# Optimization experiments

Hardware: AMD Instinct MI355X
Metric: run time of the kernel (lower is better)

Reference implementation:

```python
import jax, jax.numpy as jnp
import numpy as np

B, L, D, H, NL, DFF = 32, 64, 256, 8, 2, 2048
S, I, DSEM, DDENSE, DSPARSE = 16, 16, 128, 128, 128


def layer_norm(x, g, b, eps=1e-5):
    m = x.mean(-1, keepdims=True)
    v = ((x - m) ** 2).mean(-1, keepdims=True)
    return (x - m) / jnp.sqrt(v + eps) * g + b


def encoder_layer(x, ipw, ipb, ow, ob, g1, b1, g2, b2, f1w, f1b, f2w, f2b):
    # PyTorch TransformerEncoderLayer (post-norm, ReLU FFN, dropout inactive).
    b, t, d = x.shape
    dh = d // H
    qkv = x @ ipw.T + ipb  # (b,t,3d)
    q, k, v = jnp.split(qkv, 3, axis=-1)
    split_heads = lambda z: z.reshape(b, t, H, dh).transpose(0, 2, 1, 3)
    q, k, v = split_heads(q), split_heads(k), split_heads(v)
    att = jax.nn.softmax(jnp.einsum('bhqd,bhkd->bhqk', q, k) / np.float32(np.sqrt(dh)), axis=-1)
    o = jnp.einsum('bhqk,bhkd->bhqd', att, v).transpose(0, 2, 1, 3).reshape(b, t, d)
    x = layer_norm(x + o @ ow.T + ob, g1, b1)
    h = jax.nn.relu(x @ f1w.T + f1b) @ f2w.T + f2b
    return layer_norm(x + h, g2, b2)


def setup_inputs() -> dict:
    key = jax.random.key(0)
    ks = jax.random.split(key, 16)
    sc = np.float32(0.02)
    return dict(
        dense=jax.random.normal(ks[0], (B, L, DDENSE), jnp.float32),
        sparse=jax.random.normal(ks[1], (B, L, DSPARSE), jnp.float32),
        W_feat=jax.random.normal(ks[2], (DDENSE + DSPARSE, D), jnp.float32) * sc,
        b_feat=jnp.zeros((D,), jnp.float32),
        in_proj_w=jax.random.normal(ks[3], (NL, 3 * D, D), jnp.float32) * sc,
        in_proj_b=jnp.zeros((NL, 3 * D), jnp.float32),
        out_w=jax.random.normal(ks[4], (NL, D, D), jnp.float32) * sc,
        out_b=jnp.zeros((NL, D), jnp.float32),
        ln1_g=jnp.ones((NL, D), jnp.float32), ln1_b=jnp.zeros((NL, D), jnp.float32),
        ln2_g=jnp.ones((NL, D), jnp.float32), ln2_b=jnp.zeros((NL, D), jnp.float32),
        ff1_w=jax.random.normal(ks[5], (NL, DFF, D), jnp.float32) * sc,
        ff1_b=jnp.zeros((NL, DFF), jnp.float32),
        ff2_w=jax.random.normal(ks[6], (NL, D, DFF), jnp.float32) * sc,
        ff2_b=jnp.zeros((NL, D), jnp.float32),
        w_act=jax.random.normal(ks[7], (D, 1), jnp.float32) * sc,
        w_route_ws=jax.random.normal(ks[8], (L, S, D), jnp.float32) * sc,
        w_pose_ws=jax.random.normal(ks[9], (L, S, D, D), jnp.float32) * sc,
        w_route_si=jax.random.normal(ks[10], (S, I, D), jnp.float32) * sc,
        w_pose_si=jax.random.normal(ks[11], (S, I, D, D), jnp.float32) * sc,
        cls_w=jax.random.normal(ks[12], (DSEM, 2 * D), jnp.float32) * sc,
        cls_b=jnp.zeros((DSEM,), jnp.float32),
        inorm_g=jnp.ones((DSEM,), jnp.float32),
        inorm_b=jnp.zeros((DSEM,), jnp.float32),
    )


def reference(dense, sparse, W_feat, b_feat, in_proj_w, in_proj_b, out_w, out_b,
              ln1_g, ln1_b, ln2_g, ln2_b, ff1_w, ff1_b, ff2_w, ff2_b,
              w_act, w_route_ws, w_pose_ws, w_route_si, w_pose_si,
              cls_w, cls_b, inorm_g, inorm_b):
    # TokenFeaturizer: concat(dense, sparse) -> Linear -> (b,L,d)
    tok = jnp.concatenate([dense, sparse], axis=-1) @ W_feat + b_feat
    cls = tok.sum(axis=1, keepdims=True)  # einsum 'bld->bd' CLS token
    x = jnp.concatenate([tok, cls], axis=1)  # (b, L+1, d)
    for i in range(in_proj_w.shape[0]):
        x = encoder_layer(x, in_proj_w[i], in_proj_b[i], out_w[i], out_b[i],
                          ln1_g[i], ln1_b[i], ln2_g[i], ln2_b[i],
                          ff1_w[i], ff1_b[i], ff2_w[i], ff2_b[i])
    words, cls_tok = x[:, :L], x[:, L]  # (b,L,d), (b,d)

    # --- route words -> slots ('weighted_sig') ---
    a_words = jax.nn.sigmoid((words @ w_act)[..., 0])  # (b,L)
    c_ws = jax.nn.softmax(jnp.einsum('lsd,bld->bls', w_route_ws, words), axis=-1)
    a_num = jnp.einsum('bls,bl->bs', c_ws, a_words)
    a_slots = a_num / a_words.sum(axis=1, keepdims=True)
    u_hat = jnp.einsum('lsij,blj->blsi', w_pose_ws, words)  # (b,L,S,d)
    u_num = jnp.einsum('bls,bl,blsi->bsi', c_ws, a_words, u_hat)
    u_slots = u_num / a_num[..., None]  # (b,S,d)

    # --- route slots -> intents ---
    c_si = jax.nn.softmax(jnp.einsum('sid,bsd->bsi', w_route_si, u_slots), axis=-1)
    an = jnp.einsum('bsi,bs->bi', c_si, a_slots)
    a_intents = an / (a_slots.sum(axis=1, keepdims=True) + 1e-8)
    u_hat_i = jnp.einsum('sijk,bsk->bsik', w_pose_si, u_slots)  # (b,S,I,d)
    un = jnp.einsum('bsi,bs,bsik->bik', c_si, a_slots, u_hat_i)
    u_intents = un / (an[..., None] + 1e-8)  # (b,I,d)

    # argmax over intents, gather winning pose
    idx = jnp.argmax(a_intents, axis=-1)  # (b,)
    poses = u_intents[jnp.arange(u_intents.shape[0]), idx]  # (b,d)
    intents = jnp.concatenate([cls_tok, poses], axis=-1) @ cls_w.T + cls_b
    intents = layer_norm(intents, inorm_g, inorm_b)
    return (c_ws, intents)
```

## Files before the change

### kernel.cpp

```cpp
#include <hip/hip_runtime.h>
#include <hip/hip_bf16.h>
#include <math.h>

#define B_ 32
#define L_ 64
#define D_ 256
#define H_ 8
#define T_ 65
#define NT_ (B_*T_)
#define DFF_ 2048
#define S_ 16
#define I_ 16
#define DSEM_ 128

typedef __attribute__((ext_vector_type(8))) short bf16x8;
typedef __attribute__((ext_vector_type(4))) float f32x4;

typedef __attribute__((address_space(1))) const void gbl_void;
typedef __attribute__((address_space(3))) void lds_void;
#define GLOAD16(g, l) __builtin_amdgcn_global_load_lds((gbl_void*)(g), (lds_void*)(l), 16, 0, 0)

__device__ inline unsigned short f2bu(float f) {
  union { float f; unsigned u; } a; a.f = f;
  unsigned r = a.u + 0x7FFF + ((a.u >> 16) & 1);
  return (unsigned short)(r >> 16);
}
__device__ inline float b2f(unsigned short u) {
  union { unsigned u; float f; } a; a.u = ((unsigned)u) << 16;
  return a.f;
}

__device__ inline float wave_reduce_sum(float v) {
#pragma unroll
  for (int m = 32; m >= 1; m >>= 1) v += __shfl_xor(v, m, 64);
  return v;
}

__device__ inline float block_reduce_sum_256(float v, float* sred) {
  v = wave_reduce_sum(v);
  int tid = threadIdx.x;
  if ((tid & 63) == 0) sred[tid >> 6] = v;
  __syncthreads();
  float r = sred[0] + sred[1] + sred[2] + sred[3];
  __syncthreads();
  return r;
}

__global__ __launch_bounds__(256) void conv_fused_kernel(
    const float* __restrict__ dense, const float* __restrict__ sparse, unsigned short* __restrict__ cat,
    const float* __restrict__ wfeat, unsigned short* __restrict__ wfeatT,
    const float* __restrict__ ipw, const float* __restrict__ ow,
    const float* __restrict__ f1w, const float* __restrict__ f2w,
    unsigned short* __restrict__ ipwB, unsigned short* __restrict__ owB,
    unsigned short* __restrict__ f1wB, unsigned short* __restrict__ f2wB) {
  __shared__ float tb[64][65];
  int bid = blockIdx.x, tid = threadIdx.x;
  if (bid < 2048) {
    int idx = bid * 256 + tid;
    int r = idx >> 8, c = idx & 255;
    float v = (c < 128) ? dense[r * 128 + c] : sparse[r * 128 + (c - 128)];
    cat[idx] = f2bu(v);
  } else if (bid < 2064) {
    int blk = bid - 2048;
    int k0 = (blk & 3) * 64, n0 = (blk >> 2) * 64;
    int wid = tid >> 6, lane = tid & 63;
#pragma unroll
    for (int p = 0; p < 16; ++p)
      tb[p * 4 + wid][lane] = wfeat[(size_t)(k0 + p * 4 + wid) * 256 + n0 + lane];
    __syncthreads();
#pragma unroll
    for (int p = 0; p < 16; ++p)
      wfeatT[(size_t)(n0 + p * 4 + wid) * 256 + k0 + lane] = f2bu(tb[lane][p * 4 + wid]);
  } else {
    int i = (bid - 2064) * 256 + tid;
    const float* src; unsigned short* dst; int off;
    if (i < 98304)       { src = ipw; dst = ipwB; off = i; }
    else if (i < 131072) { src = ow;  dst = owB;  off = i - 98304; }
    else if (i < 393216) { src = f1w; dst = f1wB; off = i - 131072; }
    else                 { src = f2w; dst = f2wB; off = i - 393216; }
    float4 v = ((const float4*)src)[off];
    short4 o;
    o.x = (short)f2bu(v.x); o.y = (short)f2bu(v.y);
    o.z = (short)f2bu(v.z); o.w = (short)f2bu(v.w);
    ((short4*)dst)[off] = o;
  }
}

template <int ACT, int OUT_BF16, int NFRAG>
__global__ __launch_bounds__(256) void gemm_bf2_kernel(const unsigned short* __restrict__ A,
                                                       const unsigned short* __restrict__ W,
                                                       const float* __restrict__ bias,
                                                       float* __restrict__ Cf, unsigned short* __restrict__ Cb,
                                                       int M, int N, int K) {
  __shared__ __align__(16) unsigned short As[2][32 * 64];
  __shared__ __align__(16) unsigned short Bs[2][NFRAG * 64 * 64];
  int tid = threadIdx.x, wid = tid >> 6, lane = tid & 63;
  int row0 = blockIdx.y * 32, col0 = blockIdx.x * (64 * NFRAG);
  int lr = lane >> 3;
  int sc = ((lane & 7) ^ (lr & 7)) << 3;
  const unsigned short* Asrc = A + (size_t)(row0 + wid * 8 + lr) * K + sc;
  const unsigned short* Bsrc[2 * NFRAG];
#pragma unroll
  for (int p = 0; p < 2 * NFRAG; ++p)
    Bsrc[p] = W + (size_t)(col0 + wid * 16 * NFRAG + p * 8 + lr) * K + sc;
  unsigned short* AsW = &As[0][0] + wid * (8 * 64);
  unsigned short* BsW = &Bs[0][0] + wid * (16 * NFRAG * 64);

  f32x4 acc[2][NFRAG];
#pragma unroll
  for (int i = 0; i < 2; ++i)
#pragma unroll
    for (int j = 0; j < NFRAG; ++j) acc[i][j] = (f32x4){0.f, 0.f, 0.f, 0.f};

  GLOAD16(Asrc, AsW);
#pragma unroll
  for (int p = 0; p < 2 * NFRAG; ++p) GLOAD16(Bsrc[p], BsW + p * (8 * 64));

  int nk = K >> 6, cur = 0;
  int kg = lane >> 4, l15 = lane & 15;
  for (int kt = 0; kt < nk; ++kt) {
    __syncthreads();
    if (kt + 1 < nk) {
      int k0 = (kt + 1) << 6;
      GLOAD16(Asrc + k0, AsW + (cur ^ 1) * (32 * 64));
#pragma unroll
      for (int p = 0; p < 2 * NFRAG; ++p)
        GLOAD16(Bsrc[p] + k0, BsW + (cur ^ 1) * (NFRAG * 64 * 64) + p * (8 * 64));
    }
    const unsigned short* Ab = &As[cur][0];
    const unsigned short* Bb = &Bs[cur][0];
#pragma unroll
    for (int kk = 0; kk < 2; ++kk) {
      int cc = kk * 4 + kg;
      bf16x8 bfr[NFRAG];
#pragma unroll
      for (int fn = 0; fn < NFRAG; ++fn) {
        int rn = wid * 16 * NFRAG + fn * 16 + l15;
        bfr[fn] = *(const bf16x8*)&Bb[rn * 64 + ((cc ^ (rn & 7)) << 3)];
      }
#pragma unroll
      for (int fm = 0; fm < 2; ++fm) {
        int rm = fm * 16 + l15;
        bf16x8 afr = *(const bf16x8*)&Ab[rm * 64 + ((cc ^ (rm & 7)) << 3)];
#pragma unroll
        for (int fn = 0; fn < NFRAG; ++fn)
          acc[fm][fn] = __builtin_amdgcn_mfma_f32_16x16x32_bf16(afr, bfr[fn], acc[fm][fn], 0, 0, 0);
      }
    }
    cur ^= 1;
  }
#pragma unroll
  for (int fm = 0; fm < 2; ++fm) {
#pragma unroll
    for (int fn = 0; fn < NFRAG; ++fn) {
      int col = col0 + wid * 16 * NFRAG + fn * 16 + l15;
      float bi = bias[col];
      int rbase = row0 + fm * 16 + ((lane >> 4) << 2);
#pragma unroll
      for (int r = 0; r < 4; ++r) {
        int grow = rbase + r;
        float v = acc[fm][fn][r] + bi;
        if (ACT == 1) v = fmaxf(v, 0.f);
        if (OUT_BF16) Cb[(size_t)grow * N + col] = f2bu(v);
        else          Cf[(size_t)grow * N + col] = v;
      }
    }
  }
}

__global__ __launch_bounds__(256) void ln_residual_kernel(float* __restrict__ x, unsigned short* __restrict__ xbf,
                                                          const float* __restrict__ proj,
                                                          const float* __restrict__ g, const float* __restrict__ bb) {
  __shared__ float sred[4];
  int r = blockIdx.x, d = threadIdx.x;
  float v = x[(size_t)r * D_ + d] + proj[(size_t)r * D_ + d];
  float mean = block_reduce_sum_256(v, sred) * (1.f / 256.f);
  float dv = v - mean;
  float var = block_reduce_sum_256(dv * dv, sred) * (1.f / 256.f);
  float o = dv * (1.f / sqrtf(var + 1e-5f)) * g[d] + bb[d];
  x[(size_t)r * D_ + d] = o;
  xbf[(size_t)r * D_ + d] = f2bu(o);
}

__global__ void build_x_kernel(const float* __restrict__ tok, float* __restrict__ x,
                               unsigned short* __restrict__ xbf) {
  int b = blockIdx.x, d = threadIdx.x;
  float s = 0.f;
  for (int l = 0; l < L_; ++l) {
    float v = tok[((size_t)(b * L_ + l)) * D_ + d];
    size_t o = ((size_t)(b * T_ + l)) * D_ + d;
    x[o] = v; xbf[o] = f2bu(v);
    s += v;
  }
  size_t o = ((size_t)(b * T_ + L_)) * D_ + d;
  x[o] = s; xbf[o] = f2bu(s);
}

__global__ __launch_bounds__(256) void attn_kernel(const unsigned short* __restrict__ qkv,
                                                   unsigned short* __restrict__ attn_out) {
  int bh = blockIdx.x;
  int b = bh >> 3, h = bh & 7;
  __shared__ float Q[T_][32], K[T_][32], V[T_][32];
  __shared__ float Sc[T_][T_ + 1];
  int tid = threadIdx.x;
  for (int idx = tid; idx < T_ * 32; idx += 256) {
    int t = idx >> 5, d = idx & 31;
    const unsigned short* base = qkv + ((size_t)(b * T_ + t)) * 768 + h * 32 + d;
    Q[t][d] = b2f(base[0]);
    K[t][d] = b2f(base[256]);
    V[t][d] = b2f(base[512]);
  }
  __syncthreads();
  for (int idx = tid; idx < T_ * T_; idx += 256) {
    int qi = idx / T_, ki = idx % T_;
    float s = 0.f;
#pragma unroll
    for (int d = 0; d < 32; ++d) s += Q[qi][d] * K[ki][d];
    Sc[qi][ki] = s * 0.17677669529663687f;
  }
  __syncthreads();
  {
    int q = tid & 3;
    for (int row = tid >> 2; row < T_; row += 64) {
      float mx = -1e30f;
      for (int k = q; k < T_; k += 4) mx = fmaxf(mx, Sc[row][k]);
      mx = fmaxf(mx, __shfl_xor(mx, 1, 64));
      mx = fmaxf(mx, __shfl_xor(mx, 2, 64));
      float sum = 0.f;
      for (int k = q; k < T_; k += 4) { float e = expf(Sc[row][k] - mx); Sc[row][k] = e; sum += e; }
      sum += __shfl_xor(sum, 1, 64);
      sum += __shfl_xor(sum, 2, 64);
      float inv = 1.f / sum;
      for (int k = q; k < T_; k += 4) Sc[row][k] *= inv;
    }
  }
  __syncthreads();
  for (int idx = tid; idx < T_ * 32; idx += 256) {
    int t = idx >> 5, d = idx & 31;
    float acc = 0.f;
    for (int k = 0; k < T_; ++k) acc += Sc[t][k] * V[k][d];
    attn_out[((size_t)(b * T_ + t)) * D_ + h * 32 + d] = f2bu(acc);
  }
}

__global__ __launch_bounds__(256) void cws_kernel(const float* __restrict__ x, const float* __restrict__ w_route,
                                                  const float* __restrict__ w_act, float* __restrict__ c_ws_out,
                                                  float* __restrict__ a_words) {
  int bl = blockIdx.x;
  int b = bl >> 6, l = bl & 63;
  __shared__ float word[256];
  __shared__ float logits[16];
  __shared__ float sred[4];
  int t = threadIdx.x;
  word[t] = x[((size_t)(b * T_ + l)) * D_ + t];
  __syncthreads();
  float pa = word[t] * w_act[t];
  float asum = block_reduce_sum_256(pa, sred);
  if (t == 0) a_words[b * 64 + l] = 1.f / (1.f + expf(-asum));
  int s = t >> 4, j0 = t & 15;
  float p = 0.f;
  for (int j = j0; j < 256; j += 16) p += w_route[((size_t)(l * 16 + s)) * 256 + j] * word[j];
#pragma unroll
  for (int m = 8; m >= 1; m >>= 1) p += __shfl_xor(p, m, 64);
  if (j0 == 0) logits[s] = p;
  __syncthreads();
  if (t < 16) {
    float mx = -1e30f;
#pragma unroll
    for (int k = 0; k < 16; ++k) mx = fmaxf(mx, logits[k]);
    float sum = 0.f;
#pragma unroll
    for (int k = 0; k < 16; ++k) sum += expf(logits[k] - mx);
    c_ws_out[(size_t)bl * 16 + t] = expf(logits[t] - mx) / sum;
  }
}

__global__ __launch_bounds__(64) void slot_agg_kernel(const float* __restrict__ c_ws, const float* __restrict__ a_words,
                                                      float* __restrict__ a_num, float* __restrict__ a_slots,
                                                      float* __restrict__ asl_sum) {
  int b = blockIdx.x, lane = threadIdx.x;
  float aw = a_words[b * 64 + lane];
  float asum = wave_reduce_sum(aw);
  float inv = 1.f / asum;
  float ssum = 0.f;
  for (int s = 0; s < 16; ++s) {
    float p = c_ws[((size_t)(b * 64 + lane)) * 16 + s] * aw;
    float r = wave_reduce_sum(p);
    if (lane == 0) {
      a_num[b * 16 + s] = r;
      a_slots[b * 16 + s] = r * inv;
      ssum += r * inv;
    }
  }
  if (lane == 0) asl_sum[b] = ssum;
}

__global__ __launch_bounds__(256, 4) void pose_ws3_kernel(const unsigned short* __restrict__ xbf,
                                                          const float* __restrict__ P,
                                                          const float* __restrict__ c_ws,
                                                          const float* __restrict__ a_words,
                                                          float* __restrict__ partial) {
  int bid = blockIdx.x;
  int ih = bid & 1, s = (bid >> 1) & 15, lg = bid >> 5;
  int iBase = ih * 128;
  __shared__ __align__(16) unsigned short Bs[32 * 256];
  int tid = threadIdx.x, wid = tid >> 6, lane = tid & 63;
  int kg = lane >> 4, l15 = lane & 15;
  f32x4 acc[2][2];
#pragma unroll
  for (int i = 0; i < 2; ++i)
#pragma unroll
    for (int j = 0; j < 2; ++j) acc[i][j] = (f32x4){0.f, 0.f, 0.f, 0.f};

#pragma unroll
  for (int li = 0; li < 2; ++li) {
    int l = lg + li * 32;
    __syncthreads();
    {
      int b = tid >> 3, c0 = (tid & 7) * 4;
      float w = c_ws[((size_t)(b * 64 + l)) * 16 + s] * a_words[b * 64 + l];
      const unsigned short* src = xbf + ((size_t)(b * T_ + l)) * D_;
#pragma unroll
      for (int j = 0; j < 4; ++j) {
        int c = c0 + j;
        union { float4 f4; unsigned short u[8]; } in, out;
        in.f4 = *(const float4*)(src + c * 8);
#pragma unroll
        for (int e = 0; e < 8; ++e) out.u[e] = f2bu(w * b2f(in.u[e]));
        *(float4*)&Bs[b * 256 + ((c ^ (b & 7)) << 3)] = out.f4;
      }
    }
    __syncthreads();
    const float* Pbase = P + (((size_t)(l * 16 + s)) << 16);
#pragma unroll
    for (int k0 = 0; k0 < 256; k0 += 64) {
#pragma unroll
      for (int kk = 0; kk < 2; ++kk) {
        int cc = (k0 >> 3) + kk * 4 + kg;
        bf16x8 bfr[2];
#pragma unroll
        for (int fn = 0; fn < 2; ++fn) {
          int rb = fn * 16 + l15;
          bfr[fn] = *(const bf16x8*)&Bs[rb * 256 + ((cc ^ (rb & 7)) << 3)];
        }
        int kbase = k0 + kk * 32 + kg * 8;
#pragma unroll
        for (int fm = 0; fm < 2; ++fm) {
          int row = iBase + wid * 32 + fm * 16 + l15;
          const float* src = Pbase + (size_t)row * 256 + kbase;
          float4 v0 = *(const float4*)src;
          float4 v1 = *(const float4*)(src + 4);
          union { bf16x8 b8; unsigned short u[8]; } pk;
          pk.u[0] = f2bu(v0.x); pk.u[1] = f2bu(v0.y); pk.u[2] = f2bu(v0.z); pk.u[3] = f2bu(v0.w);
          pk.u[4] = f2bu(v1.x); pk.u[5] = f2bu(v1.y); pk.u[6] = f2bu(v1.z); pk.u[7] = f2bu(v1.w);
          acc[fm][0] = __builtin_amdgcn_mfma_f32_16x16x32_bf16(pk.b8, bfr[0], acc[fm][0], 0, 0, 0);
          acc[fm][1] = __builtin_amdgcn_mfma_f32_16x16x32_bf16(pk.b8, bfr[1], acc[fm][1], 0, 0, 0);
        }
      }
    }
  }
  float* pout = partial + ((size_t)(lg * 16 + s)) * 8192;
#pragma unroll
  for (int fm = 0; fm < 2; ++fm) {
#pragma unroll
    for (int fn = 0; fn < 2; ++fn) {
      int b = fn * 16 + l15;
      int i0 = iBase + wid * 32 + fm * 16 + (kg << 2);
#pragma unroll
      for (int r = 0; r < 4; ++r)
        pout[(i0 + r) * 32 + b] = acc[fm][fn][r];
    }
  }
}

__global__ __launch_bounds__(256) void reduce_uslots_kernel(const float* __restrict__ partial,
                                                            const float* __restrict__ a_num,
                                                            float* __restrict__ u_slots) {
  int s = blockIdx.x >> 5, ic = blockIdx.x & 31;
  int t = threadIdx.x;
  int i = ic * 8 + (t >> 5), b = t & 31;
  size_t off = (size_t)s * 8192 + i * 32 + b;
  float a0 = 0.f, a1 = 0.f, a2 = 0.f, a3 = 0.f;
#pragma unroll
  for (int lg = 0; lg < 32; lg += 4) {
    a0 += partial[((size_t)(lg + 0) * 16) * 8192 + off];
    a1 += partial[((size_t)(lg + 1) * 16) * 8192 + off];
    a2 += partial[((size_t)(lg + 2) * 16) * 8192 + off];
    a3 += partial[((size_t)(lg + 3) * 16) * 8192 + off];
  }
  u_slots[((size_t)(b * 16 + s)) * 256 + i] = (a0 + a1 + a2 + a3) / a_num[b * 16 + s];
}

__global__ __launch_bounds__(256) void csi_kernel(const float* __restrict__ u_slots, const float* __restrict__ w_route_si,
                                                  float* __restrict__ c_si) {
  int bs = blockIdx.x;
  int s = bs & 15;
  __shared__ float row[256];
  __shared__ float logits[16];
  int t = threadIdx.x;
  row[t] = u_slots[(size_t)bs * 256 + t];
  __syncthreads();
  int i = t >> 4, j0 = t & 15;
  float p = 0.f;
  for (int j = j0; j < 256; j += 16) p += w_route_si[((size_t)(s * 16 + i)) * 256 + j] * row[j];
#pragma unroll
  for (int m = 8; m >= 1; m >>= 1) p += __shfl_xor(p, m, 64);
  if (j0 == 0) logits[i] = p;
  __syncthreads();
  if (t < 16) {
    float mx = -1e30f;
#pragma unroll
    for (int k = 0; k < 16; ++k) mx = fmaxf(mx, logits[k]);
    float sum = 0.f;
#pragma unroll
    for (int k = 0; k < 16; ++k) sum += expf(logits[k] - mx);
    c_si[(size_t)bs * 16 + t] = expf(logits[t] - mx) / sum;
  }
}

__global__ void pose_si_partial_kernel(const float* __restrict__ P, float* __restrict__ R4) {
  int si = blockIdx.x >> 2, jc = blockIdx.x & 3;
  int k = threadIdx.x;
  const float* base = P + (size_t)si * 65536 + (size_t)jc * 64 * 256 + k;
  float a0 = 0.f, a1 = 0.f, a2 = 0.f, a3 = 0.f;
#pragma unroll
  for (int j = 0; j < 64; j += 4) {
    a0 += base[(j + 0) * 256];
    a1 += base[(j + 1) * 256];
    a2 += base[(j + 2) * 256];
    a3 += base[(j + 3) * 256];
  }
  R4[(size_t)jc * 65536 + si * 256 + k] = a0 + a1 + a2 + a3;
}

__global__ __launch_bounds__(256) void un_merged_kernel(const float* __restrict__ c_si,
                                                        const float* __restrict__ a_slots,
                                                        const float* __restrict__ R4,
                                                        const float* __restrict__ u_slots,
                                                        float* __restrict__ u_pose) {
  int b = blockIdx.x, t = threadIdx.x;
  __shared__ float csi_s[256];
  __shared__ float asl_s[16];
  __shared__ float an_s[16];
  __shared__ float w_s[16];
  __shared__ float an_star;
  __shared__ int istar_s;
  csi_s[t] = c_si[(size_t)b * 256 + t];
  if (t < 16) asl_s[t] = a_slots[b * 16 + t];
  __syncthreads();
  if (t < 16) {
    float acc = 0.f;
#pragma unroll
    for (int s = 0; s < 16; ++s) acc += csi_s[s * 16 + t] * asl_s[s];
    an_s[t] = acc;
  }
  __syncthreads();
  if (t == 0) {
    int best = 0;
    float bv = an_s[0];
    for (int k = 1; k < 16; ++k)
      if (an_s[k] > bv) { bv = an_s[k]; best = k; }
    istar_s = best;
    an_star = bv;
  }
  __syncthreads();
  int istar = istar_s;
  if (t < 16) w_s[t] = csi_s[t * 16 + istar] * asl_s[t];
  __syncthreads();
  float acc = 0.f;
#pragma unroll
  for (int s = 0; s < 16; ++s) {
    size_t ro = ((size_t)(s * 16 + istar)) * 256 + t;
    float r = R4[ro] + R4[65536 + ro] + R4[131072 + ro] + R4[196608 + ro];
    acc += w_s[s] * r * u_slots[((size_t)(b * 16 + s)) * 256 + t];
  }
  u_pose[(size_t)b * 256 + t] = acc / (an_star + 1e-8f);
}

__global__ __launch_bounds__(128) void final_kernel(const float* __restrict__ x, const float* __restrict__ u_pose,
                                                    const float* __restrict__ cls_w,
                                                    const float* __restrict__ cls_b, const float* __restrict__ g,
                                                    const float* __restrict__ bb, float* __restrict__ out) {
  int b = blockIdx.x, m = threadIdx.x;
  __shared__ float row[512];
  __shared__ float sred[2];
  for (int d = m; d < 256; d += 128) {
    row[d] = x[((size_t)(b * T_ + L_)) * D_ + d];
    row[256 + d] = u_pose[(size_t)b * 256 + d];
  }
  __syncthreads();
  float acc = cls_b[m];
  for (int j = 0; j < 512; ++j) acc += cls_w[(size_t)m * 512 + j] * row[j];
  float v = wave_reduce_sum(acc);
  if ((m & 63) == 0) sred[m >> 6] = v;
  __syncthreads();
  float mean = (sred[0] + sred[1]) * (1.f / 128.f);
  __syncthreads();
  float dv = acc - mean;
  float v2 = wave_reduce_sum(dv * dv);
  if ((m & 63) == 0) sred[m >> 6] = v2;
  __syncthreads();
  float var = (sred[0] + sred[1]) * (1.f / 128.f);
  out[(size_t)b * 128 + m] = dv * (1.f / sqrtf(var + 1e-5f)) * g[m] + bb[m];
}

extern "C" void kernel_launch(void* const* d_in, const int* in_sizes, int n_in,
                              void* d_out, int out_size, void* d_ws, size_t ws_size,
                              hipStream_t stream) {
  (void)in_sizes; (void)n_in; (void)out_size; (void)ws_size;
  const float* dense      = (const float*)d_in[0];
  const float* sparse     = (const float*)d_in[1];
  const float* W_feat     = (const float*)d_in[2];
  const float* b_feat     = (const float*)d_in[3];
  const float* in_proj_w  = (const float*)d_in[4];
  const float* in_proj_b  = (const float*)d_in[5];
  const float* out_w      = (const float*)d_in[6];
  const float* out_b      = (const float*)d_in[7];
  const float* ln1_g      = (const float*)d_in[8];
  const float* ln1_b      = (const float*)d_in[9];
  const float* ln2_g      = (const float*)d_in[10];
  const float* ln2_b      = (const float*)d_in[11];
  const float* ff1_w      = (const float*)d_in[12];
  const float* ff1_b      = (const float*)d_in[13];
  const float* ff2_w      = (const float*)d_in[14];
  const float* ff2_b      = (const float*)d_in[15];
  const float* w_act      = (const float*)d_in[16];
  const float* w_route_ws = (const float*)d_in[17];
  const float* w_pose_ws  = (const float*)d_in[18];
  const float* w_route_si = (const float*)d_in[19];
  const float* w_pose_si  = (const float*)d_in[20];
  const float* cls_w      = (const float*)d_in[21];
  const float* cls_b      = (const float*)d_in[22];
  const float* inorm_g    = (const float*)d_in[23];
  const float* inorm_b    = (const float*)d_in[24];

  float* ws = (float*)d_ws;
  float* X       = ws;
  float* PROJ    = X + 532480;
  float* a_words = PROJ + 532480;
  float* a_num   = a_words + 2048;
  float* a_slots = a_num + 512;
  float* asl_sum = a_slots + 512;
  float* u_slots = asl_sum + 32;
  float* c_si    = u_slots + 131072;
  float* u_pose  = c_si + 8192;
  float* R4      = u_pose + 8192;

  unsigned short* bfb   = (unsigned short*)(R4 + 262144);
  unsigned short* Xbf   = bfb;
  unsigned short* QKVbf = Xbf + 532480;
  unsigned short* HAR   = QKVbf + 1597440;
  unsigned short* CATbf = HAR;
  unsigned short* ATTNbf= HAR + 2097152;
  unsigned short* wfeatT= HAR + 4259840;
  unsigned short* ipwB  = wfeatT + 65536;
  unsigned short* owB   = ipwB + 393216;
  unsigned short* f1wB  = owB + 131072;
  unsigned short* f2wB  = f1wB + 1048576;
  float* partial = (float*)QKVbf;

  float* c_ws_out    = (float*)d_out;
  float* intents_out = (float*)d_out + 32768;

  conv_fused_kernel<<<4624, 256, 0, stream>>>(dense, sparse, CATbf, W_feat, wfeatT,
                                              in_proj_w, out_w, ff1_w, ff2_w,
                                              ipwB, owB, f1wB, f2wB);

  gemm_bf2_kernel<0, 0, 1><<<dim3(4, 64), 256, 0, stream>>>(CATbf, wfeatT, b_feat, PROJ, nullptr, 2048, 256, 256);
  build_x_kernel<<<32, 256, 0, stream>>>(PROJ, X, Xbf);

  for (int layer = 0; layer < 2; ++layer) {
    const unsigned short* ipw = ipwB + (size_t)layer * 196608;
    const unsigned short* ow  = owB + (size_t)layer * 65536;
    const unsigned short* f1w = f1wB + (size_t)layer * 524288;
    const unsigned short* f2w = f2wB + (size_t)layer * 524288;
    const float* ipb = in_proj_b + (size_t)layer * 768;
    const float* ob  = out_b + (size_t)layer * 256;
    const float* g1  = ln1_g + (size_t)layer * 256;
    const float* b1  = ln1_b + (size_t)layer * 256;
    const float* g2  = ln2_g + (size_t)layer * 256;
    const float* b2  = ln2_b + (size_t)layer * 256;
    const float* f1b = ff1_b + (size_t)layer * DFF_;
    const float* f2b = ff2_b + (size_t)layer * 256;

    gemm_bf2_kernel<0, 1, 2><<<dim3(6, 65), 256, 0, stream>>>(Xbf, ipw, ipb, nullptr, QKVbf, NT_, 768, 256);
    attn_kernel<<<B_ * H_, 256, 0, stream>>>(QKVbf, ATTNbf);
    gemm_bf2_kernel<0, 0, 1><<<dim3(4, 65), 256, 0, stream>>>(ATTNbf, ow, ob, PROJ, nullptr, NT_, 256, 256);
    ln_residual_kernel<<<NT_, 256, 0, stream>>>(X, Xbf, PROJ, g1, b1);
    gemm_bf2_kernel<1, 1, 2><<<dim3(16, 65), 256, 0, stream>>>(Xbf, f1w, f1b, nullptr, HAR, NT_, DFF_, 256);
    gemm_bf2_kernel<0, 0, 1><<<dim3(4, 65), 256, 0, stream>>>(HAR, f2w, f2b, PROJ, nullptr, NT_, 256, 2048);
    ln_residual_kernel<<<NT_, 256, 0, stream>>>(X, Xbf, PROJ, g2, b2);
  }

  cws_kernel<<<2048, 256, 0, stream>>>(X, w_route_ws, w_act, c_ws_out, a_words);
  slot_agg_kernel<<<32, 64, 0, stream>>>(c_ws_out, a_words, a_num, a_slots, asl_sum);
  pose_ws3_kernel<<<1024, 256, 0, stream>>>(Xbf, w_pose_ws, c_ws_out, a_words, partial);
  reduce_uslots_kernel<<<512, 256, 0, stream>>>(partial, a_num, u_slots);
  pose_si_partial_kernel<<<1024, 256, 0, stream>>>(w_pose_si, R4);
  csi_kernel<<<512, 256, 0, stream>>>(u_slots, w_route_si, c_si);
  un_merged_kernel<<<32, 256, 0, stream>>>(c_si, a_slots, R4, u_slots, u_pose);
  final_kernel<<<32, 128, 0, stream>>>(X, u_pose, cls_w, cls_b, inorm_g, inorm_b, intents_out);
}
```

Measured before the change: 279.3 us.

## Split attention by query halves, fuse pose kernels, merge capsule tail kernels

Attention now launches two blocks per (batch, head), each handling half the query rows, to double parallelism. The pose_si reduction is folded into the pose_ws kernel as extra blocks, and its inner loop is restructured to prefetch the next fp32 weight chunk before converting and running the current MFMA step. The csi, un_merged and final kernels are merged into one per-batch tail kernel. Together these aim to cut launch count and improve latency hiding, at the cost of K/V loads being repeated across the attention halves and a larger single-block tail.

```diff
diff --git a/kernel.cpp b/kernel.cpp
--- a/kernel.cpp
+++ b/kernel.cpp
@@ -198,20 +198,24 @@
 
 __global__ __launch_bounds__(256) void attn_kernel(const unsigned short* __restrict__ qkv,
                                                    unsigned short* __restrict__ attn_out) {
-  int bh = blockIdx.x;
+  int bid = blockIdx.x;
+  int half = bid & 1;
+  int bh = bid >> 1;
   int b = bh >> 3, h = bh & 7;
-  __shared__ float Q[T_][32], K[T_][32], V[T_][32];
-  __shared__ float Sc[T_][T_ + 1];
+  int t0 = half ? 33 : 0;
+  int nrows = half ? 32 : 33;
+  __shared__ float Q[33][32], K[T_][32], V[T_][32];
+  __shared__ float Sc[33][T_ + 1];
   int tid = threadIdx.x;
   for (int idx = tid; idx < T_ * 32; idx += 256) {
     int t = idx >> 5, d = idx & 31;
     const unsigned short* base = qkv + ((size_t)(b * T_ + t)) * 768 + h * 32 + d;
-    Q[t][d] = b2f(base[0]);
     K[t][d] = b2f(base[256]);
     V[t][d] = b2f(base[512]);
-  }
-  __syncthreads();
-  for (int idx = tid; idx < T_ * T_; idx += 256) {
+    if (t >= t0 && t < t0 + nrows) Q[t - t0][d] = b2f(base[0]);
+  }
+  __syncthreads();
+  for (int idx = tid; idx < nrows * T_; idx += 256) {
     int qi = idx / T_, ki = idx % T_;
     float s = 0.f;
 #pragma unroll
@@ -221,7 +225,7 @@
   __syncthreads();
   {
     int q = tid & 3;
-    for (int row = tid >> 2; row < T_; row += 64) {
+    for (int row = tid >> 2; row < nrows; row += 64) {
       float mx = -1e30f;
       for (int k = q; k < T_; k += 4) mx = fmaxf(mx, Sc[row][k]);
       mx = fmaxf(mx, __shfl_xor(mx, 1, 64));
@@ -235,11 +239,11 @@
     }
   }
   __syncthreads();
-  for (int idx = tid; idx < T_ * 32; idx += 256) {
+  for (int idx = tid; idx < nrows * 32; idx += 256) {
     int t = idx >> 5, d = idx & 31;
     float acc = 0.f;
     for (int k = 0; k < T_; ++k) acc += Sc[t][k] * V[k][d];
-    attn_out[((size_t)(b * T_ + t)) * D_ + h * 32 + d] = f2bu(acc);
+    attn_out[((size_t)(b * T_ + t0 + t)) * D_ + h * 32 + d] = f2bu(acc);
   }
 }
 
@@ -295,16 +299,34 @@
   if (lane == 0) asl_sum[b] = ssum;
 }
 
-__global__ __launch_bounds__(256, 4) void pose_ws3_kernel(const unsigned short* __restrict__ xbf,
-                                                          const float* __restrict__ P,
-                                                          const float* __restrict__ c_ws,
-                                                          const float* __restrict__ a_words,
-                                                          float* __restrict__ partial) {
-  int bid = blockIdx.x;
+__global__ __launch_bounds__(256, 4) void pose_fused_kernel(const unsigned short* __restrict__ xbf,
+                                                            const float* __restrict__ P,
+                                                            const float* __restrict__ c_ws,
+                                                            const float* __restrict__ a_words,
+                                                            float* __restrict__ partial,
+                                                            const float* __restrict__ Psi,
+                                                            float* __restrict__ R4) {
+  int bid = blockIdx.x, tid = threadIdx.x;
+  if (bid >= 1024) {
+    int idx = bid - 1024;
+    int si = idx >> 2, jc = idx & 3;
+    int k = tid;
+    const float* base = Psi + (size_t)si * 65536 + (size_t)jc * 64 * 256 + k;
+    float a0 = 0.f, a1 = 0.f, a2 = 0.f, a3 = 0.f;
+#pragma unroll
+    for (int j = 0; j < 64; j += 4) {
+      a0 += base[(j + 0) * 256];
+      a1 += base[(j + 1) * 256];
+      a2 += base[(j + 2) * 256];
+      a3 += base[(j + 3) * 256];
+    }
+    R4[(size_t)jc * 65536 + si * 256 + k] = a0 + a1 + a2 + a3;
+    return;
+  }
   int ih = bid & 1, s = (bid >> 1) & 15, lg = bid >> 5;
   int iBase = ih * 128;
   __shared__ __align__(16) unsigned short Bs[32 * 256];
-  int tid = threadIdx.x, wid = tid >> 6, lane = tid & 63;
+  int wid = tid >> 6, lane = tid & 63;
   int kg = lane >> 4, l15 = lane & 15;
   f32x4 acc[2][2];
 #pragma unroll
@@ -312,6 +334,7 @@
 #pragma unroll
     for (int j = 0; j < 2; ++j) acc[i][j] = (f32x4){0.f, 0.f, 0.f, 0.f};
 
+  int r0 = iBase + wid * 32 + l15;
 #pragma unroll
   for (int li = 0; li < 2; ++li) {
     int l = lg + li * 32;
@@ -332,31 +355,38 @@
     }
     __syncthreads();
     const float* Pbase = P + (((size_t)(l * 16 + s)) << 16);
-#pragma unroll
-    for (int k0 = 0; k0 < 256; k0 += 64) {
-#pragma unroll
-      for (int kk = 0; kk < 2; ++kk) {
-        int cc = (k0 >> 3) + kk * 4 + kg;
-        bf16x8 bfr[2];
-#pragma unroll
-        for (int fn = 0; fn < 2; ++fn) {
-          int rb = fn * 16 + l15;
-          bfr[fn] = *(const bf16x8*)&Bs[rb * 256 + ((cc ^ (rb & 7)) << 3)];
-        }
-        int kbase = k0 + kk * 32 + kg * 8;
-#pragma unroll
-        for (int fm = 0; fm < 2; ++fm) {
-          int row = iBase + wid * 32 + fm * 16 + l15;
-          const float* src = Pbase + (size_t)row * 256 + kbase;
-          float4 v0 = *(const float4*)src;
-          float4 v1 = *(const float4*)(src + 4);
-          union { bf16x8 b8; unsigned short u[8]; } pk;
-          pk.u[0] = f2bu(v0.x); pk.u[1] = f2bu(v0.y); pk.u[2] = f2bu(v0.z); pk.u[3] = f2bu(v0.w);
-          pk.u[4] = f2bu(v1.x); pk.u[5] = f2bu(v1.y); pk.u[6] = f2bu(v1.z); pk.u[7] = f2bu(v1.w);
-          acc[fm][0] = __builtin_amdgcn_mfma_f32_16x16x32_bf16(pk.b8, bfr[0], acc[fm][0], 0, 0, 0);
-          acc[fm][1] = __builtin_amdgcn_mfma_f32_16x16x32_bf16(pk.b8, bfr[1], acc[fm][1], 0, 0, 0);
-        }
+    const float* pr0 = Pbase + (size_t)r0 * 256 + kg * 8;
+    const float* pr1 = pr0 + 16 * 256;
+    float4 c00 = *(const float4*)(pr0);
+    float4 c01 = *(const float4*)(pr0 + 4);
+    float4 c10 = *(const float4*)(pr1);
+    float4 c11 = *(const float4*)(pr1 + 4);
+#pragma unroll
+    for (int step = 0; step < 8; ++step) {
+      float4 n00, n01, n10, n11;
+      if (step < 7) {
+        const float* q0 = pr0 + (step + 1) * 32;
+        const float* q1 = pr1 + (step + 1) * 32;
+        n00 = *(const float4*)(q0); n01 = *(const float4*)(q0 + 4);
+        n10 = *(const float4*)(q1); n11 = *(const float4*)(q1 + 4);
       }
+      int cc = 4 * step + kg;
+      bf16x8 bfr[2];
+#pragma unroll
+      for (int fn = 0; fn < 2; ++fn) {
+        int rb = fn * 16 + l15;
+        bfr[fn] = *(const bf16x8*)&Bs[rb * 256 + ((cc ^ (rb & 7)) << 3)];
+      }
+      union { bf16x8 b8; unsigned short u[8]; } pk0, pk1;
+      pk0.u[0] = f2bu(c00.x); pk0.u[1] = f2bu(c00.y); pk0.u[2] = f2bu(c00.z); pk0.u[3] = f2bu(c00.w);
+      pk0.u[4] = f2bu(c01.x); pk0.u[5] = f2bu(c01.y); pk0.u[6] = f2bu(c01.z); pk0.u[7] = f2bu(c01.w);
+      pk1.u[0] = f2bu(c10.x); pk1.u[1] = f2bu(c10.y); pk1.u[2] = f2bu(c10.z); pk1.u[3] = f2bu(c10.w);
+      pk1.u[4] = f2bu(c11.x); pk1.u[5] = f2bu(c11.y); pk1.u[6] = f2bu(c11.z); pk1.u[7] = f2bu(c11.w);
+      acc[0][0] = __builtin_amdgcn_mfma_f32_16x16x32_bf16(pk0.b8, bfr[0], acc[0][0], 0, 0, 0);
+      acc[0][1] = __builtin_amdgcn_mfma_f32_16x16x32_bf16(pk0.b8, bfr[1], acc[0][1], 0, 0, 0);
+      acc[1][0] = __builtin_amdgcn_mfma_f32_16x16x32_bf16(pk1.b8, bfr[0], acc[1][0], 0, 0, 0);
+      acc[1][1] = __builtin_amdgcn_mfma_f32_16x16x32_bf16(pk1.b8, bfr[1], acc[1][1], 0, 0, 0);
+      c00 = n00; c01 = n01; c10 = n10; c11 = n11;
     }
   }
   float* pout = partial + ((size_t)(lg * 16 + s)) * 8192;
@@ -391,117 +421,102 @@
   u_slots[((size_t)(b * 16 + s)) * 256 + i] = (a0 + a1 + a2 + a3) / a_num[b * 16 + s];
 }
 
-__global__ __launch_bounds__(256) void csi_kernel(const float* __restrict__ u_slots, const float* __restrict__ w_route_si,
-                                                  float* __restrict__ c_si) {
-  int bs = blockIdx.x;
-  int s = bs & 15;
-  __shared__ float row[256];
-  __shared__ float logits[16];
-  int t = threadIdx.x;
-  row[t] = u_slots[(size_t)bs * 256 + t];
-  __syncthreads();
-  int i = t >> 4, j0 = t & 15;
-  float p = 0.f;
-  for (int j = j0; j < 256; j += 16) p += w_route_si[((size_t)(s * 16 + i)) * 256 + j] * row[j];
-#pragma unroll
-  for (int m = 8; m >= 1; m >>= 1) p += __shfl_xor(p, m, 64);
-  if (j0 == 0) logits[i] = p;
+__global__ __launch_bounds__(256) void cap_tail_kernel(const float* __restrict__ u_slots,
+                                                       const float* __restrict__ a_slots,
+                                                       const float* __restrict__ w_route_si,
+                                                       const float* __restrict__ R4,
+                                                       const float* __restrict__ x,
+                                                       const float* __restrict__ cls_w,
+                                                       const float* __restrict__ cls_b,
+                                                       const float* __restrict__ g,
+                                                       const float* __restrict__ bb,
+                                                       float* __restrict__ out) {
+  int b = blockIdx.x, t = threadIdx.x;
+  __shared__ float us[16][256];
+  __shared__ float lg_s[16][17];
+  __shared__ float asl_s[16], an_s[16], w_s[16];
+  __shared__ float row[512];
+  __shared__ float part[256];
+  __shared__ float sredx[4];
+  __shared__ float an_star_s;
+  __shared__ int istar_s;
+#pragma unroll
+  for (int p = 0; p < 16; ++p) us[p][t] = u_slots[((size_t)(b * 16 + p)) * 256 + t];
+  if (t < 16) asl_s[t] = a_slots[b * 16 + t];
+  __syncthreads();
+  int i4 = t >> 4, j0 = t & 15;
+  for (int s = 0; s < 16; ++s) {
+    float p = 0.f;
+    for (int j = j0; j < 256; j += 16) p += w_route_si[((size_t)(s * 16 + i4)) * 256 + j] * us[s][j];
+#pragma unroll
+    for (int m = 8; m >= 1; m >>= 1) p += __shfl_xor(p, m, 64);
+    if (j0 == 0) lg_s[s][i4] = p;
+  }
   __syncthreads();
   if (t < 16) {
     float mx = -1e30f;
 #pragma unroll
-    for (int k = 0; k < 16; ++k) mx = fmaxf(mx, logits[k]);
+    for (int i = 0; i < 16; ++i) mx = fmaxf(mx, lg_s[t][i]);
     float sum = 0.f;
 #pragma unroll
-    for (int k = 0; k < 16; ++k) sum += expf(logits[k] - mx);
-    c_si[(size_t)bs * 16 + t] = expf(logits[t] - mx) / sum;
-  }
-}
-
-__global__ void pose_si_partial_kernel(const float* __restrict__ P, float* __restrict__ R4) {
-  int si = blockIdx.x >> 2, jc = blockIdx.x & 3;
-  int k = threadIdx.x;
-  const float* base = P + (size_t)si * 65536 + (size_t)jc * 64 * 256 + k;
-  float a0 = 0.f, a1 = 0.f, a2 = 0.f, a3 = 0.f;
-#pragma unroll
-  for (int j = 0; j < 64; j += 4) {
-    a0 += base[(j + 0) * 256];
-    a1 += base[(j + 1) * 256];
-    a2 += base[(j + 2) * 256];
-    a3 += base[(j + 3) * 256];
-  }
-  R4[(size_t)jc * 65536 + si * 256 + k] = a0 + a1 + a2 + a3;
-}
-
-__global__ __launch_bounds__(256) void un_merged_kernel(const float* __restrict__ c_si,
-                                                        const float* __restrict__ a_slots,
-                                                        const float* __restrict__ R4,
-                                                        const float* __restrict__ u_slots,
-                                                        float* __restrict__ u_pose) {
-  int b = blockIdx.x, t = threadIdx.x;
-  __shared__ float csi_s[256];
-  __shared__ float asl_s[16];
-  __shared__ float an_s[16];
-  __shared__ float w_s[16];
-  __shared__ float an_star;
-  __shared__ int istar_s;
-  csi_s[t] = c_si[(size_t)b * 256 + t];
-  if (t < 16) asl_s[t] = a_slots[b * 16 + t];
+    for (int i = 0; i < 16; ++i) { float e = expf(lg_s[t][i] - mx); lg_s[t][i] = e; sum += e; }
+    float inv = 1.f / sum;
+#pragma unroll
+    for (int i = 0; i < 16; ++i) lg_s[t][i] *= inv;
+  }
   __syncthreads();
   if (t < 16) {
-    float acc = 0.f;
-#pragma unroll
-    for (int s = 0; s < 16; ++s) acc += csi_s[s * 16 + t] * asl_s[s];
-    an_s[t] = acc;
+    float a = 0.f;
+#pragma unroll
+    for (int s = 0; s < 16; ++s) a += lg_s[s][t] * asl_s[s];
+    an_s[t] = a;
   }
   __syncthreads();
   if (t == 0) {
-    int best = 0;
-    float bv = an_s[0];
+    int best = 0; float bv = an_s[0];
+#pragma unroll
     for (int k = 1; k < 16; ++k)
       if (an_s[k] > bv) { bv = an_s[k]; best = k; }
-    istar_s = best;
-    an_star = bv;
+    istar_s = best; an_star_s = bv;
   }
   __syncthreads();
   int istar = istar_s;
-  if (t < 16) w_s[t] = csi_s[t * 16 + istar] * asl_s[t];
-  __syncthreads();
-  float acc = 0.f;
-#pragma unroll
-  for (int s = 0; s < 16; ++s) {
-    size_t ro = ((size_t)(s * 16 + istar)) * 256 + t;
-    float r = R4[ro] + R4[65536 + ro] + R4[131072 + ro] + R4[196608 + ro];
-    acc += w_s[s] * r * u_slots[((size_t)(b * 16 + s)) * 256 + t];
-  }
-  u_pose[(size_t)b * 256 + t] = acc / (an_star + 1e-8f);
-}
-
-__global__ __launch_bounds__(128) void final_kernel(const float* __restrict__ x, const float* __restrict__ u_pose,
-                                                    const float* __restrict__ cls_w,
-                                                    const float* __restrict__ cls_b, const float* __restrict__ g,
-                                                    const float* __restrict__ bb, float* __restrict__ out) {
-  int b = blockIdx.x, m = threadIdx.x;
-  __shared__ float row[512];
-  __shared__ float sred[2];
-  for (int d = m; d < 256; d += 128) {
-    row[d] = x[((size_t)(b * T_ + L_)) * D_ + d];
-    row[256 + d] = u_pose[(size_t)b * 256 + d];
-  }
-  __syncthreads();
-  float acc = cls_b[m];
-  for (int j = 0; j < 512; ++j) acc += cls_w[(size_t)m * 512 + j] * row[j];
-  float v = wave_reduce_sum(acc);
-  if ((m & 63) == 0) sred[m >> 6] = v;
-  __syncthreads();
-  float mean = (sred[0] + sred[1]) * (1.f / 128.f);
-  __syncthreads();
-  float dv = acc - mean;
-  float v2 = wave_reduce_sum(dv * dv);
-  if ((m & 63) == 0) sred[m >> 6] = v2;
-  __syncthreads();
-  float var = (sred[0] + sred[1]) * (1.f / 128.f);
-  out[(size_t)b * 128 + m] = dv * (1.f / sqrtf(var + 1e-5f)) * g[m] + bb[m];
+  if (t < 16) w_s[t] = lg_s[t][istar] * asl_s[t];
+  __syncthreads();
+  {
+    float acc = 0.f;
+#pragma unroll
+    for (int s = 0; s < 16; ++s) {
+      size_t ro = ((size_t)(s * 16 + istar)) * 256 + t;
+      float r = R4[ro] + R4[65536 + ro] + R4[131072 + ro] + R4[196608 + ro];
+      acc += w_s[s] * r * us[s][t];
+    }
+    row[256 + t] = acc / (an_star_s + 1e-8f);
+    row[t] = x[((size_t)(b * T_ + L_)) * D_ + t];
+  }
+  __syncthreads();
+  {
+    int m = t & 127, hf = t >> 7;
+    const float* wr = cls_w + (size_t)m * 512 + hf * 256;
+    const float* rr = &row[hf * 256];
+    float acc = 0.f;
+    for (int j = 0; j < 256; ++j) acc += wr[j] * rr[j];
+    part[t] = acc;
+  }
+  __syncthreads();
+  float a = (t < 128) ? part[t] + part[t + 128] + cls_b[t] : 0.f;
+  float v = wave_reduce_sum(a);
+  if ((t & 63) == 0) sredx[t >> 6] = v;
+  __syncthreads();
+  float mean = (sredx[0] + sredx[1] + sredx[2] + sredx[3]) * (1.f / 128.f);
+  float dv = a - mean;
+  float q = (t < 128) ? dv * dv : 0.f;
+  float v2 = wave_reduce_sum(q);
+  if ((t & 63) == 0) sredx[t >> 6] = v2;
+  __syncthreads();
+  float var = (sredx[0] + sredx[1] + sredx[2] + sredx[3]) * (1.f / 128.f);
+  if (t < 128)
+    out[(size_t)b * 128 + t] = dv * (1.f / sqrtf(var + 1e-5f)) * g[t] + bb[t];
 }
 
 extern "C" void kernel_launch(void* const* d_in, const int* in_sizes, int n_in,
@@ -542,9 +557,7 @@
   float* a_slots = a_num + 512;
   float* asl_sum = a_slots + 512;
   float* u_slots = asl_sum + 32;
-  float* c_si    = u_slots + 131072;
-  float* u_pose  = c_si + 8192;
-  float* R4      = u_pose + 8192;
+  float* R4      = u_slots + 131072;
 
   unsigned short* bfb   = (unsigned short*)(R4 + 262144);
   unsigned short* Xbf   = bfb;
@@ -584,7 +597,7 @@
     const float* f2b = ff2_b + (size_t)layer * 256;
 
     gemm_bf2_kernel<0, 1, 2><<<dim3(6, 65), 256, 0, stream>>>(Xbf, ipw, ipb, nullptr, QKVbf, NT_, 768, 256);
-    attn_kernel<<<B_ * H_, 256, 0, stream>>>(QKVbf, ATTNbf);
+    attn_kernel<<<B_ * H_ * 2, 256, 0, stream>>>(QKVbf, ATTNbf);
     gemm_bf2_kernel<0, 0, 1><<<dim3(4, 65), 256, 0, stream>>>(ATTNbf, ow, ob, PROJ, nullptr, NT_, 256, 256);
     ln_residual_kernel<<<NT_, 256, 0, stream>>>(X, Xbf, PROJ, g1, b1);
     gemm_bf2_kernel<1, 1, 2><<<dim3(16, 65), 256, 0, stream>>>(Xbf, f1w, f1b, nullptr, HAR, NT_, DFF_, 256);
@@ -594,10 +607,9 @@
 
   cws_kernel<<<2048, 256, 0, stream>>>(X, w_route_ws, w_act, c_ws_out, a_words);
   slot_agg_kernel<<<32, 64, 0, stream>>>(c_ws_out, a_words, a_num, a_slots, asl_sum);
-  pose_ws3_kernel<<<1024, 256, 0, stream>>>(Xbf, w_pose_ws, c_ws_out, a_words, partial);
+  pose_fused_kernel<<<2048, 256, 0, stream>>>(Xbf, w_pose_ws, c_ws_out, a_words, partial,
+                                              w_pose_si, R4);
   reduce_uslots_kernel<<<512, 256, 0, stream>>>(partial, a_num, u_slots);
-  pose_si_partial_kernel<<<1024, 256, 0, stream>>>(w_pose_si, R4);
-  csi_kernel<<<512, 256, 0, stream>>>(u_slots, w_route_si, c_si);
-  un_merged_kernel<<<32, 256, 0, stream>>>(c_si, a_slots, R4, u_slots, u_pose);
-  final_kernel<<<32, 128, 0, stream>>>(X, u_pose, cls_w, cls_b, inorm_g, inorm_b, intents_out);
-}
+  cap_tail_kernel<<<32, 256, 0, stream>>>(u_slots, a_slots, w_route_si, R4, X,
+                                          cls_w, cls_b, inorm_g, inorm_b, intents_out);
+}
```

Result: slower. 317.2 us (+13.6%).
